# Kernel optimization log

Hardware: AMD Instinct MI355X
Metric: run time of the kernel (lower is better)

The kernel has to match this reference:

```python
import jax, jax.numpy as jnp
import numpy as np

B, CIN, COUT, HID, H, W, K, PAD = 16, 64, 64, 32, 32, 32, 5, 2


def self_attention(x, Wq, Wk, Wv):
    # x: [B,C,H,W]; Wq,Wk: [HID,C]; Wv: [C,C]  (1x1 convs as channel matmuls)
    b, c, h, w = x.shape
    n = h * w
    xf = x.reshape(b, c, n)                      # [B,C,N]
    q = jnp.einsum('dc,bcn->bdn', Wq, xf)        # [B,HID,N]
    k = jnp.einsum('dc,bcn->bdn', Wk, xf)        # [B,HID,N]
    v = jnp.einsum('ec,bcn->ben', Wv, xf)        # [B,C,N]
    scores = jnp.einsum('bdn,bdm->bnm', q, k)    # [B,N,N]
    attn = jax.nn.softmax(scores, axis=-1)
    out = jnp.einsum('bcm,bnm->bcn', v, attn)    # aggregate values
    out = out.reshape(b, c, h, w)
    return x + out, attn                          # residual


def conv_lstm_cell(x, h, c, W_lstm, b_lstm):
    combined = jnp.concatenate([x, h], axis=1)   # [B,CIN+COUT,H,W]
    gates = jax.lax.conv_general_dilated(
        combined, W_lstm, window_strides=(1, 1),
        padding=[(PAD, PAD), (PAD, PAD)],
        dimension_numbers=('NCHW', 'OIHW', 'NCHW'))
    gates = gates + b_lstm[None, :, None, None]
    i, f, o, g = jnp.split(gates, 4, axis=1)
    i, f, o = jax.nn.sigmoid(i), jax.nn.sigmoid(f), jax.nn.sigmoid(o)
    g = jnp.tanh(g)
    c_new = f * c + i * g
    h_new = o * jnp.tanh(c_new)
    return h_new, c_new


def setup_inputs() -> dict:
    key = jax.random.key(0)
    ks = jax.random.split(key, 12)
    s = 0.05
    return {
        'x': jax.random.normal(ks[0], (B, CIN, H, W), jnp.float32),
        'h': jax.random.normal(ks[1], (B, COUT, H, W), jnp.float32),
        'c': jax.random.normal(ks[2], (B, COUT, H, W), jnp.float32),
        'Wq_x': jax.random.normal(ks[3], (HID, CIN), jnp.float32) * s,
        'Wk_x': jax.random.normal(ks[4], (HID, CIN), jnp.float32) * s,
        'Wv_x': jax.random.normal(ks[5], (CIN, CIN), jnp.float32) * s,
        'Wq_h': jax.random.normal(ks[6], (HID, COUT), jnp.float32) * s,
        'Wk_h': jax.random.normal(ks[7], (HID, COUT), jnp.float32) * s,
        'Wv_h': jax.random.normal(ks[8], (COUT, COUT), jnp.float32) * s,
        'W_lstm': jax.random.normal(ks[9], (4 * COUT, CIN + COUT, K, K), jnp.float32) * s,
        'b_lstm': jnp.zeros((4 * COUT,), jnp.float32),
    }


def reference(x, h, c, Wq_x, Wk_x, Wv_x, Wq_h, Wk_h, Wv_h, W_lstm, b_lstm):
    X, _ = self_attention(x, Wq_x, Wk_x, Wv_x)
    new_h, new_c = conv_lstm_cell(X, h, c, W_lstm, b_lstm)
    new_h, atten = self_attention(new_h, Wq_h, Wk_h, Wv_h)
    new_h = new_h + new_h  # faithful to `new_h += new_h`
    return new_h, new_c, atten
```

## Files before the change

### kernel.cpp

```cpp
#include <hip/hip_runtime.h>
#include <hip/hip_bf16.h>
#include <cstddef>
#include <cstdint>

#define NTOK 1024
#define NB   16
#define NC   64
#define NHID 32

#define PAD_BSTRIDE 165888
#define PAD_KSTRIDE 82944
#define PAD_BYTES   5308416

typedef __attribute__((ext_vector_type(8))) short short8;
typedef __attribute__((ext_vector_type(4))) float f32x4;

__device__ __forceinline__ ushort f2b(float f) {
  uint32_t u = __builtin_bit_cast(uint32_t, f);
  return (ushort)((u + 0x7FFFu + ((u >> 16) & 1u)) >> 16);
}
__device__ __forceinline__ float b2f(ushort u) {
  return __builtin_bit_cast(float, (uint32_t)u << 16);
}

__global__ __launch_bounds__(256) void tpose_bf16_kernel(
    const float* __restrict__ src, ushort* __restrict__ dst, int padded) {
  __shared__ float tile[64][65];
  int t = threadIdx.x;
  int n0 = blockIdx.x * 64, b = blockIdx.y;
  const float* s = src + (size_t)b * NC * NTOK;
#pragma unroll
  for (int r = 0; r < 4; ++r) {
    int c = r * 16 + (t >> 4);
    int nl = (t & 15) * 4;
    float4 v = *(const float4*)(s + (size_t)c * NTOK + n0 + nl);
    tile[c][nl] = v.x; tile[c][nl + 1] = v.y; tile[c][nl + 2] = v.z; tile[c][nl + 3] = v.w;
  }
  __syncthreads();
  int tok = t >> 2, c0 = (t & 3) * 16;
  __attribute__((aligned(16))) ushort tmp[16];
#pragma unroll
  for (int i = 0; i < 16; ++i) tmp[i] = f2b(tile[c0 + i][tok]);
  int gtok = n0 + tok;
  ushort* d;
  if (padded)
    d = dst + (size_t)b * PAD_BSTRIDE + ((gtok >> 5) + 2) * 2304 + ((gtok & 31) + 2) * 64 + c0;
  else
    d = dst + ((size_t)b * NTOK + gtok) * NC + c0;
  *(uint4*)(d)     = *(const uint4*)(tmp);
  *(uint4*)(d + 8) = *(const uint4*)(tmp + 8);
}

__global__ __launch_bounds__(256) void wqkv_pre_kernel(
    const float* __restrict__ Wq, const float* __restrict__ Wk,
    const float* __restrict__ Wv, ushort* __restrict__ wqb,
    ushort* __restrict__ wkb, ushort* __restrict__ wvb) {
  int i = blockIdx.x * 256 + threadIdx.x;
  if (i < 2048) { wqb[i] = f2b(Wq[i]); wkb[i] = f2b(Wk[i]); }
  wvb[i] = f2b(Wv[i]);
}

__global__ __launch_bounds__(256) void qkvproj_kernel(
    const ushort* __restrict__ xT, const ushort* __restrict__ wqb,
    const ushort* __restrict__ wkb, const ushort* __restrict__ wvb,
    ushort* __restrict__ qT, ushort* __restrict__ kT, ushort* __restrict__ vb) {
  __shared__ ushort sq[64][32], sk[64][32];
  int t = threadIdx.x, wave = t >> 6, lane = t & 63;
  int lo = lane & 15, lg = lane >> 4;
  int n0 = blockIdx.x * 64, b = blockIdx.y;
  int nw = n0 + wave * 16;
  const ushort* xrow = xT + ((size_t)b * NTOK + nw + lo) * NC + 8 * lg;
  short8 a0 = *(const short8*)(xrow);
  short8 a1 = *(const short8*)(xrow + 32);
  f32x4 aq[2], ak[2];
#pragma unroll
  for (int dg = 0; dg < 2; ++dg) {
    const ushort* wq = wqb + (size_t)(dg * 16 + lo) * NC + 8 * lg;
    const ushort* wk = wkb + (size_t)(dg * 16 + lo) * NC + 8 * lg;
    f32x4 z = {0.f, 0.f, 0.f, 0.f};
    aq[dg] = __builtin_amdgcn_mfma_f32_16x16x32_bf16(a0, *(const short8*)(wq), z, 0, 0, 0);
    aq[dg] = __builtin_amdgcn_mfma_f32_16x16x32_bf16(a1, *(const short8*)(wq + 32), aq[dg], 0, 0, 0);
    ak[dg] = __builtin_amdgcn_mfma_f32_16x16x32_bf16(a0, *(const short8*)(wk), z, 0, 0, 0);
    ak[dg] = __builtin_amdgcn_mfma_f32_16x16x32_bf16(a1, *(const short8*)(wk + 32), ak[dg], 0, 0, 0);
  }
  f32x4 av[4];
#pragma unroll
  for (int g = 0; g < 4; ++g) {
    const ushort* wv = wvb + (size_t)(g * 16 + lo) * NC + 8 * lg;
    f32x4 z = {0.f, 0.f, 0.f, 0.f};
    av[g] = __builtin_amdgcn_mfma_f32_16x16x32_bf16(*(const short8*)(wv), a0, z, 0, 0, 0);
    av[g] = __builtin_amdgcn_mfma_f32_16x16x32_bf16(*(const short8*)(wv + 32), a1, av[g], 0, 0, 0);
  }
#pragma unroll
  for (int dg = 0; dg < 2; ++dg)
#pragma unroll
    for (int r = 0; r < 4; ++r) {
      sq[wave * 16 + 4 * lg + r][dg * 16 + lo] = f2b(aq[dg][r]);
      sk[wave * 16 + 4 * lg + r][dg * 16 + lo] = f2b(ak[dg][r]);
    }
  ushort* vbase = vb + (size_t)b * NC * NTOK + nw + lo;
#pragma unroll
  for (int g = 0; g < 4; ++g)
#pragma unroll
    for (int r = 0; r < 4; ++r)
      vbase[(size_t)(g * 16 + lg * 4 + r) * NTOK] = f2b(av[g][r]);
  __syncthreads();
  int tok = t >> 2, d0 = (t & 3) * 8;
  size_t base = ((size_t)b * NTOK + n0 + tok) * NHID + d0;
  *(short8*)(qT + base) = *(const short8*)(&sq[tok][d0]);
  *(short8*)(kT + base) = *(const short8*)(&sk[tok][d0]);
}

#define SP 1048
template <bool ATTN2>
__global__ __launch_bounds__(256) void attn_fused_kernel(
    const ushort* __restrict__ qT, const ushort* __restrict__ kT,
    const ushort* __restrict__ vb, const float* __restrict__ resid,
    float* __restrict__ attnf, float* __restrict__ outf,
    ushort* __restrict__ outb_pad, float scale) {
  __shared__ ushort s_lds[16 * SP];
  __shared__ float wmax[4][16], wsum[4][16];
  int t = threadIdx.x, wave = t >> 6, lane = t & 63;
  int lo = lane & 15, lg = lane >> 4;
  int n0 = blockIdx.x * 16, b = blockIdx.y;
  int m0 = wave * 256;
  short8 a = *(const short8*)(qT + ((size_t)b * NTOK + n0 + lo) * NHID + 8 * lg);
  f32x4 acc[16];
#pragma unroll
  for (int j = 0; j < 16; ++j) {
    short8 bf = *(const short8*)(kT + ((size_t)b * NTOK + m0 + j * 16 + lo) * NHID + 8 * lg);
    f32x4 z = {0.f, 0.f, 0.f, 0.f};
    acc[j] = __builtin_amdgcn_mfma_f32_16x16x32_bf16(a, bf, z, 0, 0, 0);
  }
  float pm[4];
#pragma unroll
  for (int r = 0; r < 4; ++r) {
    float m = acc[0][r];
#pragma unroll
    for (int j = 1; j < 16; ++j) m = fmaxf(m, acc[j][r]);
#pragma unroll
    for (int off = 1; off < 16; off <<= 1) m = fmaxf(m, __shfl_xor(m, off, 64));
    pm[r] = m;
  }
  if (lo == 0)
#pragma unroll
    for (int r = 0; r < 4; ++r) wmax[wave][4 * lg + r] = pm[r];
  __syncthreads();
  float mr[4];
#pragma unroll
  for (int r = 0; r < 4; ++r)
    mr[r] = fmaxf(fmaxf(wmax[0][4 * lg + r], wmax[1][4 * lg + r]),
                  fmaxf(wmax[2][4 * lg + r], wmax[3][4 * lg + r]));
  float ps[4] = {0.f, 0.f, 0.f, 0.f};
#pragma unroll
  for (int j = 0; j < 16; ++j)
#pragma unroll
    for (int r = 0; r < 4; ++r) {
      float e = __expf(acc[j][r] - mr[r]);
      acc[j][r] = e;
      ps[r] += e;
    }
#pragma unroll
  for (int r = 0; r < 4; ++r)
#pragma unroll
    for (int off = 1; off < 16; off <<= 1) ps[r] += __shfl_xor(ps[r], off, 64);
  if (lo == 0)
#pragma unroll
    for (int r = 0; r < 4; ++r) wsum[wave][4 * lg + r] = ps[r];
  __syncthreads();
  float inv[4];
#pragma unroll
  for (int r = 0; r < 4; ++r)
    inv[r] = 1.f / (wsum[0][4 * lg + r] + wsum[1][4 * lg + r] +
                    wsum[2][4 * lg + r] + wsum[3][4 * lg + r]);
#pragma unroll
  for (int j = 0; j < 16; ++j)
#pragma unroll
    for (int r = 0; r < 4; ++r)
      s_lds[(4 * lg + r) * SP + m0 + j * 16 + lo] = f2b(acc[j][r] * inv[r]);
  __syncthreads();
  if constexpr (ATTN2) {
    int ml = lane * 4;
    float* abase = attnf + ((size_t)b * NTOK + n0) * NTOK + m0;
#pragma unroll
    for (int n = 0; n < 16; ++n) {
      ushort4 sv = *(const ushort4*)(s_lds + n * SP + m0 + ml);
      float4 o;
      o.x = b2f(sv.x); o.y = b2f(sv.y); o.z = b2f(sv.z); o.w = b2f(sv.w);
      *(float4*)(abase + (size_t)n * NTOK + ml) = o;
    }
  }
  int cb = wave * 16;
  const ushort* vbb = vb + ((size_t)b * NC + cb + lo) * NTOK;
  f32x4 acc2 = {0.f, 0.f, 0.f, 0.f}, acc3 = {0.f, 0.f, 0.f, 0.f};
  for (int ms = 0; ms < NTOK; ms += 64) {
    short8 af0 = *(const short8*)(s_lds + lo * SP + ms + 8 * lg);
    short8 bf0 = *(const short8*)(vbb + ms + 8 * lg);
    short8 af1 = *(const short8*)(s_lds + lo * SP + ms + 32 + 8 * lg);
    short8 bf1 = *(const short8*)(vbb + ms + 32 + 8 * lg);
    acc2 = __builtin_amdgcn_mfma_f32_16x16x32_bf16(af0, bf0, acc2, 0, 0, 0);
    acc3 = __builtin_amdgcn_mfma_f32_16x16x32_bf16(af1, bf1, acc3, 0, 0, 0);
  }
#pragma unroll
  for (int r = 0; r < 4; ++r) acc2[r] += acc3[r];
  int c = cb + lo;
  float4 rv = *(const float4*)(resid + ((size_t)b * NC + c) * NTOK + n0 + 4 * lg);
  float rvv[4] = {rv.x, rv.y, rv.z, rv.w};
  if constexpr (ATTN2) {
    float4 o;
    o.x = scale * (rvv[0] + acc2[0]); o.y = scale * (rvv[1] + acc2[1]);
    o.z = scale * (rvv[2] + acc2[2]); o.w = scale * (rvv[3] + acc2[3]);
    *(float4*)(outf + ((size_t)b * NC + c) * NTOK + n0 + 4 * lg) = o;
  } else {
#pragma unroll
    for (int r = 0; r < 4; ++r) {
      int tok = n0 + 4 * lg + r;
      float val = scale * (rvv[r] + acc2[r]);
      outb_pad[(size_t)b * PAD_BSTRIDE + ((tok >> 5) + 2) * 2304 +
               ((tok & 31) + 2) * 64 + c] = f2b(val);
    }
  }
}

__global__ __launch_bounds__(256) void wpre_kernel(
    const float* __restrict__ W, ushort* __restrict__ Wb) {
  int idx = blockIdx.x * 256 + threadIdx.x;
  int oc = idx >> 7, ic = idx & 127;
  const float* src = W + (size_t)idx * 25;
#pragma unroll
  for (int kk = 0; kk < 25; ++kk)
    Wb[((size_t)oc * 25 + kk) * 128 + ic] = f2b(src[kk]);
}

#define AP 76
#define BP 76
__global__ __launch_bounds__(512, 1) void conv_mfma_kernel(
    const ushort* __restrict__ pad,
    const ushort* __restrict__ Wb,
    float* __restrict__ gates0, float* __restrict__ gates1) {
  __shared__ ushort ldsA[2][256 * AP];
  __shared__ ushort ldsB[288 * BP];
  int t = threadIdx.x;
  int lane = t & 63, lo = lane & 15, lg = lane >> 4;
  int wid = t >> 6, oc_g = wid & 3, px_g = wid >> 2;
  int rp = blockIdx.x, kh = blockIdx.y, b = blockIdx.z;
  const ushort* padKH = pad + (size_t)b * PAD_BSTRIDE + (size_t)kh * PAD_KSTRIDE
                        + (size_t)(rp * 4) * 2304;

  for (int i = t; i < 2304; i += 512) {
    int pxw = i >> 3, ch8 = (i & 7) * 8;
    uint4 v = *(const uint4*)(padKH + (size_t)pxw * 64 + ch8);
    *(uint4*)(ldsB + pxw * BP + ch8) = v;
  }

  const ushort *wsrc0, *wsrc1, *wsrc2, *wsrc3;
  int adst0, adst1, adst2, adst3;
  {
    int i0 = t, i1 = 512 + t, i2 = 1024 + t, i3 = 1536 + t;
    wsrc0 = Wb + (size_t)(i0 >> 3) * 3200 + kh * 64 + (i0 & 7) * 8;
    wsrc1 = Wb + (size_t)(i1 >> 3) * 3200 + kh * 64 + (i1 & 7) * 8;
    wsrc2 = Wb + (size_t)(i2 >> 3) * 3200 + kh * 64 + (i2 & 7) * 8;
    wsrc3 = Wb + (size_t)(i3 >> 3) * 3200 + kh * 64 + (i3 & 7) * 8;
    adst0 = (i0 >> 3) * AP + (i0 & 7) * 8;
    adst1 = (i1 >> 3) * AP + (i1 & 7) * 8;
    adst2 = (i2 >> 3) * AP + (i2 & 7) * 8;
    adst3 = (i3 >> 3) * AP + (i3 & 7) * 8;
  }
  uint4 w0 = *(const uint4*)(wsrc0);
  uint4 w1 = *(const uint4*)(wsrc1);
  uint4 w2 = *(const uint4*)(wsrc2);
  uint4 w3 = *(const uint4*)(wsrc3);

  f32x4 acc[4][4];
#pragma unroll
  for (int i = 0; i < 4; ++i)
#pragma unroll
    for (int j = 0; j < 4; ++j) acc[i][j] = {0.f, 0.f, 0.f, 0.f};

  __syncthreads();
  *(uint4*)(&ldsA[0][adst0]) = w0;
  *(uint4*)(&ldsA[0][adst1]) = w1;
  *(uint4*)(&ldsA[0][adst2]) = w2;
  *(uint4*)(&ldsA[0][adst3]) = w3;
  w0 = *(const uint4*)(wsrc0 + 128);
  w1 = *(const uint4*)(wsrc1 + 128);
  w2 = *(const uint4*)(wsrc2 + 128);
  w3 = *(const uint4*)(wsrc3 + 128);
  __syncthreads();

  for (int kk = 0; kk < 25; ++kk) {
    int cur = kk & 1;
    if (kk < 24) {
      int nxt = cur ^ 1;
      *(uint4*)(&ldsA[nxt][adst0]) = w0;
      *(uint4*)(&ldsA[nxt][adst1]) = w1;
      *(uint4*)(&ldsA[nxt][adst2]) = w2;
      *(uint4*)(&ldsA[nxt][adst3]) = w3;
      int kkn = (kk < 23) ? kk + 2 : 24;
      w0 = *(const uint4*)(wsrc0 + kkn * 128);
      w1 = *(const uint4*)(wsrc1 + kkn * 128);
      w2 = *(const uint4*)(wsrc2 + kkn * 128);
      w3 = *(const uint4*)(wsrc3 + kkn * 128);
    }
    int ky = kk / 5, kx = kk - 5 * ky;
    int tapoff = (ky * 36 + kx) * BP;
#pragma unroll
    for (int icc = 0; icc < 2; ++icc) {
      short8 af[4], bf[4];
#pragma unroll
      for (int i = 0; i < 4; ++i)
        af[i] = *(const short8*)(&ldsA[cur][(oc_g * 64 + i * 16 + lo) * AP + icc * 32 + 8 * lg]);
#pragma unroll
      for (int j = 0; j < 4; ++j) {
        int pxw = (px_g * 2 + (j >> 1)) * 36 + (j & 1) * 16 + lo;
        bf[j] = *(const short8*)(ldsB + tapoff + pxw * BP + icc * 32 + 8 * lg);
      }
#pragma unroll
      for (int i = 0; i < 4; ++i)
#pragma unroll
        for (int j = 0; j < 4; ++j)
          acc[i][j] = __builtin_amdgcn_mfma_f32_16x16x32_bf16(af[i], bf[j], acc[i][j], 0, 0, 0);
    }
    __syncthreads();
  }

  float* gp = kh ? gates1 : gates0;
#pragma unroll
  for (int i = 0; i < 4; ++i)
#pragma unroll
    for (int j = 0; j < 4; ++j)
#pragma unroll
      for (int r = 0; r < 4; ++r) {
        int oc = oc_g * 64 + i * 16 + lg * 4 + r;
        int p  = rp * 128 + px_g * 64 + j * 16 + lo;
        gp[(size_t)(b * 256 + oc) * NTOK + p] = acc[i][j][r];
      }
}

__global__ __launch_bounds__(256) void lstm_kernel(
    const float* __restrict__ g0, const float* __restrict__ g1,
    const float* __restrict__ bias, const float* __restrict__ c_in,
    float* __restrict__ c_out, float* __restrict__ h_out) {
  size_t idx = (size_t)blockIdx.x * 256 + threadIdx.x;
  size_t b = idx >> 16;
  size_t r = idx & 65535;
  int ocr = (int)(r >> 10);
  size_t gbo = b * (size_t)(256 * NTOK);
  float iv = g0[gbo + r]          + g1[gbo + r]          + bias[ocr];
  float fv = g0[gbo + 65536 + r]  + g1[gbo + 65536 + r]  + bias[64 + ocr];
  float ov = g0[gbo + 131072 + r] + g1[gbo + 131072 + r] + bias[128 + ocr];
  float gv = g0[gbo + 196608 + r] + g1[gbo + 196608 + r] + bias[192 + ocr];
  iv = 1.f / (1.f + expf(-iv));
  fv = 1.f / (1.f + expf(-fv));
  ov = 1.f / (1.f + expf(-ov));
  gv = tanhf(gv);
  float cn = fv * c_in[idx] + iv * gv;
  c_out[idx] = cn;
  h_out[idx] = ov * tanhf(cn);
}

extern "C" void kernel_launch(void* const* d_in, const int* in_sizes, int n_in,
                              void* d_out, int out_size, void* d_ws, size_t ws_size,
                              hipStream_t stream) {
  const float* x      = (const float*)d_in[0];
  const float* h      = (const float*)d_in[1];
  const float* c      = (const float*)d_in[2];
  const float* Wq_x   = (const float*)d_in[3];
  const float* Wk_x   = (const float*)d_in[4];
  const float* Wv_x   = (const float*)d_in[5];
  const float* Wq_h   = (const float*)d_in[6];
  const float* Wk_h   = (const float*)d_in[7];
  const float* Wv_h   = (const float*)d_in[8];
  const float* W_lstm = (const float*)d_in[9];
  const float* b_lstm = (const float*)d_in[10];

  float* out   = (float*)d_out;
  float* new_h = out;
  float* new_c = out + 1048576;
  float* atten = out + 2097152;

  ushort* wsu = (ushort*)d_ws;
  ushort* qT  = wsu;
  ushort* kT  = wsu + 524288;
  ushort* vb  = wsu + 1048576;
  ushort* xT  = wsu + 2097152;
  ushort* wqb = wsu + 3145728;
  ushort* wkb = wsu + 3147776;
  ushort* wvb = wsu + 3149824;

  float*  gates0 = atten;
  float*  gates1 = atten + 4194304;
  ushort* Wb     = (ushort*)(atten + 8388608);
  ushort* pad    = (ushort*)(atten + 9437184);
  float*  h_mid  = new_h;

  dim3 blk(256);
  hipMemsetAsync(pad, 0, PAD_BYTES, stream);
  tpose_bf16_kernel<<<dim3(16, NB), blk, 0, stream>>>(x, xT, 0);
  wqkv_pre_kernel<<<16, blk, 0, stream>>>(Wq_x, Wk_x, Wv_x, wqb, wkb, wvb);
  qkvproj_kernel<<<dim3(16, NB), blk, 0, stream>>>(xT, wqb, wkb, wvb, qT, kT, vb);
  attn_fused_kernel<false><<<dim3(64, NB), blk, 0, stream>>>(
      qT, kT, vb, x, nullptr, nullptr, pad , 1.0f);
  wpre_kernel<<<128, blk, 0, stream>>>(W_lstm, Wb);
  tpose_bf16_kernel<<<dim3(16, NB), blk, 0, stream>>>(h, pad + PAD_KSTRIDE, 1);
  conv_mfma_kernel<<<dim3(8, 2, NB), 512, 0, stream>>>(pad, Wb, gates0, gates1);
  lstm_kernel<<<4096, blk, 0, stream>>>(gates0, gates1, b_lstm, c, new_c, h_mid);
  tpose_bf16_kernel<<<dim3(16, NB), blk, 0, stream>>>(h_mid, xT, 0);
  wqkv_pre_kernel<<<16, blk, 0, stream>>>(Wq_h, Wk_h, Wv_h, wqb, wkb, wvb);
  qkvproj_kernel<<<dim3(16, NB), blk, 0, stream>>>(xT, wqb, wkb, wvb, qT, kT, vb);
  attn_fused_kernel<true><<<dim3(64, NB), blk, 0, stream>>>(
      qT, kT, vb, h_mid, atten, new_h, nullptr, 2.0f);
}
```

Measured before the change: 131.5 us.

## Fuse LSTM gating into conv kernel and fold transpose/weight cast into QKV projection

The conv kernel now covers both input halves (x-attention and h) in one 50-step K loop over a two-row pixel tile, and applies bias, sigmoid/tanh and the cell update in its epilogue. This removes the two gate buffers and the separate LSTM kernel. The QKV projection kernel now transposes and casts its fp32 input and weights itself, which removes the transpose and weight-precast launches. The trade-off is a larger LDS footprint for the B tile, and the conv grid changes from 8x2 to 16 tiles per batch with half the pixel work per block. The fast exp-based activations may differ slightly in precision.

```diff
diff --git a/kernel.cpp b/kernel.cpp
--- a/kernel.cpp
+++ b/kernel.cpp
@@ -22,9 +22,23 @@
 __device__ __forceinline__ float b2f(ushort u) {
   return __builtin_bit_cast(float, (uint32_t)u << 16);
 }
-
-__global__ __launch_bounds__(256) void tpose_bf16_kernel(
-    const float* __restrict__ src, ushort* __restrict__ dst, int padded) {
+__device__ __forceinline__ short8 ldw8(const float* __restrict__ p) {
+  float4 f0 = *(const float4*)p, f1 = *(const float4*)(p + 4);
+  short8 r;
+  r[0] = (short)f2b(f0.x); r[1] = (short)f2b(f0.y);
+  r[2] = (short)f2b(f0.z); r[3] = (short)f2b(f0.w);
+  r[4] = (short)f2b(f1.x); r[5] = (short)f2b(f1.y);
+  r[6] = (short)f2b(f1.z); r[7] = (short)f2b(f1.w);
+  return r;
+}
+__device__ __forceinline__ float sigm(float x) { return 1.f / (1.f + __expf(-x)); }
+__device__ __forceinline__ float tanh_fast(float x) {
+  float e = __expf(2.f * x);
+  return 1.f - 2.f / (e + 1.f);
+}
+
+__global__ __launch_bounds__(256) void tpose_pad_kernel(
+    const float* __restrict__ src, ushort* __restrict__ dst) {
   __shared__ float tile[64][65];
   int t = threadIdx.x;
   int n0 = blockIdx.x * 64, b = blockIdx.y;
@@ -42,54 +56,64 @@
 #pragma unroll
   for (int i = 0; i < 16; ++i) tmp[i] = f2b(tile[c0 + i][tok]);
   int gtok = n0 + tok;
-  ushort* d;
-  if (padded)
-    d = dst + (size_t)b * PAD_BSTRIDE + ((gtok >> 5) + 2) * 2304 + ((gtok & 31) + 2) * 64 + c0;
-  else
-    d = dst + ((size_t)b * NTOK + gtok) * NC + c0;
+  ushort* d = dst + (size_t)b * PAD_BSTRIDE +
+              ((gtok >> 5) + 2) * 2304 + ((gtok & 31) + 2) * 64 + c0;
   *(uint4*)(d)     = *(const uint4*)(tmp);
   *(uint4*)(d + 8) = *(const uint4*)(tmp + 8);
 }
 
-__global__ __launch_bounds__(256) void wqkv_pre_kernel(
-    const float* __restrict__ Wq, const float* __restrict__ Wk,
-    const float* __restrict__ Wv, ushort* __restrict__ wqb,
-    ushort* __restrict__ wkb, ushort* __restrict__ wvb) {
-  int i = blockIdx.x * 256 + threadIdx.x;
-  if (i < 2048) { wqb[i] = f2b(Wq[i]); wkb[i] = f2b(Wk[i]); }
-  wvb[i] = f2b(Wv[i]);
-}
-
 __global__ __launch_bounds__(256) void qkvproj_kernel(
-    const ushort* __restrict__ xT, const ushort* __restrict__ wqb,
-    const ushort* __restrict__ wkb, const ushort* __restrict__ wvb,
+    const float* __restrict__ x, const float* __restrict__ Wq,
+    const float* __restrict__ Wk, const float* __restrict__ Wv,
     ushort* __restrict__ qT, ushort* __restrict__ kT, ushort* __restrict__ vb) {
+  __shared__ float tile[64][65];
+  __shared__ ushort xb[64][72];
   __shared__ ushort sq[64][32], sk[64][32];
   int t = threadIdx.x, wave = t >> 6, lane = t & 63;
   int lo = lane & 15, lg = lane >> 4;
   int n0 = blockIdx.x * 64, b = blockIdx.y;
-  int nw = n0 + wave * 16;
-  const ushort* xrow = xT + ((size_t)b * NTOK + nw + lo) * NC + 8 * lg;
+  const float* s = x + (size_t)b * NC * NTOK;
+#pragma unroll
+  for (int r = 0; r < 4; ++r) {
+    int c = r * 16 + (t >> 4);
+    int nl = (t & 15) * 4;
+    float4 v = *(const float4*)(s + (size_t)c * NTOK + n0 + nl);
+    tile[c][nl] = v.x; tile[c][nl + 1] = v.y; tile[c][nl + 2] = v.z; tile[c][nl + 3] = v.w;
+  }
+  __syncthreads();
+  {
+    int tok = t >> 2, c0 = (t & 3) * 16;
+    __attribute__((aligned(16))) ushort tmp[16];
+#pragma unroll
+    for (int i = 0; i < 16; ++i) tmp[i] = f2b(tile[c0 + i][tok]);
+    *(uint4*)(&xb[tok][c0])     = *(const uint4*)(tmp);
+    *(uint4*)(&xb[tok][c0 + 8]) = *(const uint4*)(tmp + 8);
+  }
+  __syncthreads();
+  const ushort* xrow = &xb[wave * 16 + lo][8 * lg];
   short8 a0 = *(const short8*)(xrow);
   short8 a1 = *(const short8*)(xrow + 32);
   f32x4 aq[2], ak[2];
 #pragma unroll
   for (int dg = 0; dg < 2; ++dg) {
-    const ushort* wq = wqb + (size_t)(dg * 16 + lo) * NC + 8 * lg;
-    const ushort* wk = wkb + (size_t)(dg * 16 + lo) * NC + 8 * lg;
+    short8 wq0 = ldw8(Wq + (size_t)(dg * 16 + lo) * NC + 8 * lg);
+    short8 wq1 = ldw8(Wq + (size_t)(dg * 16 + lo) * NC + 32 + 8 * lg);
+    short8 wk0 = ldw8(Wk + (size_t)(dg * 16 + lo) * NC + 8 * lg);
+    short8 wk1 = ldw8(Wk + (size_t)(dg * 16 + lo) * NC + 32 + 8 * lg);
     f32x4 z = {0.f, 0.f, 0.f, 0.f};
-    aq[dg] = __builtin_amdgcn_mfma_f32_16x16x32_bf16(a0, *(const short8*)(wq), z, 0, 0, 0);
-    aq[dg] = __builtin_amdgcn_mfma_f32_16x16x32_bf16(a1, *(const short8*)(wq + 32), aq[dg], 0, 0, 0);
-    ak[dg] = __builtin_amdgcn_mfma_f32_16x16x32_bf16(a0, *(const short8*)(wk), z, 0, 0, 0);
-    ak[dg] = __builtin_amdgcn_mfma_f32_16x16x32_bf16(a1, *(const short8*)(wk + 32), ak[dg], 0, 0, 0);
+    aq[dg] = __builtin_amdgcn_mfma_f32_16x16x32_bf16(a0, wq0, z, 0, 0, 0);
+    aq[dg] = __builtin_amdgcn_mfma_f32_16x16x32_bf16(a1, wq1, aq[dg], 0, 0, 0);
+    ak[dg] = __builtin_amdgcn_mfma_f32_16x16x32_bf16(a0, wk0, z, 0, 0, 0);
+    ak[dg] = __builtin_amdgcn_mfma_f32_16x16x32_bf16(a1, wk1, ak[dg], 0, 0, 0);
   }
   f32x4 av[4];
 #pragma unroll
   for (int g = 0; g < 4; ++g) {
-    const ushort* wv = wvb + (size_t)(g * 16 + lo) * NC + 8 * lg;
+    short8 wv0 = ldw8(Wv + (size_t)(g * 16 + lo) * NC + 8 * lg);
+    short8 wv1 = ldw8(Wv + (size_t)(g * 16 + lo) * NC + 32 + 8 * lg);
     f32x4 z = {0.f, 0.f, 0.f, 0.f};
-    av[g] = __builtin_amdgcn_mfma_f32_16x16x32_bf16(*(const short8*)(wv), a0, z, 0, 0, 0);
-    av[g] = __builtin_amdgcn_mfma_f32_16x16x32_bf16(*(const short8*)(wv + 32), a1, av[g], 0, 0, 0);
+    av[g] = __builtin_amdgcn_mfma_f32_16x16x32_bf16(wv0, a0, z, 0, 0, 0);
+    av[g] = __builtin_amdgcn_mfma_f32_16x16x32_bf16(wv1, a1, av[g], 0, 0, 0);
   }
 #pragma unroll
   for (int dg = 0; dg < 2; ++dg)
@@ -98,7 +122,7 @@
       sq[wave * 16 + 4 * lg + r][dg * 16 + lo] = f2b(aq[dg][r]);
       sk[wave * 16 + 4 * lg + r][dg * 16 + lo] = f2b(ak[dg][r]);
     }
-  ushort* vbase = vb + (size_t)b * NC * NTOK + nw + lo;
+  ushort* vbase = vb + (size_t)b * NC * NTOK + n0 + wave * 16 + lo;
 #pragma unroll
   for (int g = 0; g < 4; ++g)
 #pragma unroll
@@ -225,42 +249,42 @@
 __global__ __launch_bounds__(256) void wpre_kernel(
     const float* __restrict__ W, ushort* __restrict__ Wb) {
   int idx = blockIdx.x * 256 + threadIdx.x;
-  int oc = idx >> 7, ic = idx & 127;
   const float* src = W + (size_t)idx * 25;
 #pragma unroll
   for (int kk = 0; kk < 25; ++kk)
-    Wb[((size_t)oc * 25 + kk) * 128 + ic] = f2b(src[kk]);
+    Wb[((size_t)(idx >> 7) * 25 + kk) * 128 + (idx & 127)] = f2b(src[kk]);
 }
 
 #define AP 76
 #define BP 76
-__global__ __launch_bounds__(512, 1) void conv_mfma_kernel(
+__global__ __launch_bounds__(512, 1) void conv_lstm_kernel(
     const ushort* __restrict__ pad,
     const ushort* __restrict__ Wb,
-    float* __restrict__ gates0, float* __restrict__ gates1) {
+    const float* __restrict__ bias, const float* __restrict__ c_in,
+    float* __restrict__ c_out, float* __restrict__ h_out) {
   __shared__ ushort ldsA[2][256 * AP];
-  __shared__ ushort ldsB[288 * BP];
+  __shared__ ushort ldsB[432 * BP];
   int t = threadIdx.x;
   int lane = t & 63, lo = lane & 15, lg = lane >> 4;
-  int wid = t >> 6, oc_g = wid & 3, px_g = wid >> 2;
-  int rp = blockIdx.x, kh = blockIdx.y, b = blockIdx.z;
-  const ushort* padKH = pad + (size_t)b * PAD_BSTRIDE + (size_t)kh * PAD_KSTRIDE
-                        + (size_t)(rp * 4) * 2304;
-
-  for (int i = t; i < 2304; i += 512) {
-    int pxw = i >> 3, ch8 = (i & 7) * 8;
-    uint4 v = *(const uint4*)(padKH + (size_t)pxw * 64 + ch8);
-    *(uint4*)(ldsB + pxw * BP + ch8) = v;
-  }
-
+  int wid = t >> 6, ocr_base = (wid & 3) * 16, ph = wid >> 2;
+  int pt = blockIdx.x, b = blockIdx.y;
+  {
+    const ushort* pb = pad + (size_t)b * PAD_BSTRIDE + (size_t)(pt * 2) * 2304;
+    for (int i = t; i < 432 * 8; i += 512) {
+      int pxw = i >> 3, ch8 = (i & 7) * 8;
+      int kh = pxw >= 216, w = pxw - kh * 216;
+      uint4 v = *(const uint4*)(pb + (size_t)kh * PAD_KSTRIDE + w * 64 + ch8);
+      *(uint4*)(ldsB + pxw * BP + ch8) = v;
+    }
+  }
   const ushort *wsrc0, *wsrc1, *wsrc2, *wsrc3;
   int adst0, adst1, adst2, adst3;
   {
     int i0 = t, i1 = 512 + t, i2 = 1024 + t, i3 = 1536 + t;
-    wsrc0 = Wb + (size_t)(i0 >> 3) * 3200 + kh * 64 + (i0 & 7) * 8;
-    wsrc1 = Wb + (size_t)(i1 >> 3) * 3200 + kh * 64 + (i1 & 7) * 8;
-    wsrc2 = Wb + (size_t)(i2 >> 3) * 3200 + kh * 64 + (i2 & 7) * 8;
-    wsrc3 = Wb + (size_t)(i3 >> 3) * 3200 + kh * 64 + (i3 & 7) * 8;
+    wsrc0 = Wb + (size_t)(i0 >> 3) * 3200 + (i0 & 7) * 8;
+    wsrc1 = Wb + (size_t)(i1 >> 3) * 3200 + (i1 & 7) * 8;
+    wsrc2 = Wb + (size_t)(i2 >> 3) * 3200 + (i2 & 7) * 8;
+    wsrc3 = Wb + (size_t)(i3 >> 3) * 3200 + (i3 & 7) * 8;
     adst0 = (i0 >> 3) * AP + (i0 & 7) * 8;
     adst1 = (i1 >> 3) * AP + (i1 & 7) * 8;
     adst2 = (i2 >> 3) * AP + (i2 & 7) * 8;
@@ -271,11 +295,11 @@
   uint4 w2 = *(const uint4*)(wsrc2);
   uint4 w3 = *(const uint4*)(wsrc3);
 
-  f32x4 acc[4][4];
+  f32x4 acc[4][2];
 #pragma unroll
   for (int i = 0; i < 4; ++i)
 #pragma unroll
-    for (int j = 0; j < 4; ++j) acc[i][j] = {0.f, 0.f, 0.f, 0.f};
+    for (int j = 0; j < 2; ++j) acc[i][j] = {0.f, 0.f, 0.f, 0.f};
 
   __syncthreads();
   *(uint4*)(&ldsA[0][adst0]) = w0;
@@ -288,75 +312,58 @@
   w3 = *(const uint4*)(wsrc3 + 128);
   __syncthreads();
 
-  for (int kk = 0; kk < 25; ++kk) {
-    int cur = kk & 1;
-    if (kk < 24) {
+  for (int s = 0; s < 50; ++s) {
+    int cur = s & 1;
+    if (s < 49) {
       int nxt = cur ^ 1;
       *(uint4*)(&ldsA[nxt][adst0]) = w0;
       *(uint4*)(&ldsA[nxt][adst1]) = w1;
       *(uint4*)(&ldsA[nxt][adst2]) = w2;
       *(uint4*)(&ldsA[nxt][adst3]) = w3;
-      int kkn = (kk < 23) ? kk + 2 : 24;
-      w0 = *(const uint4*)(wsrc0 + kkn * 128);
-      w1 = *(const uint4*)(wsrc1 + kkn * 128);
-      w2 = *(const uint4*)(wsrc2 + kkn * 128);
-      w3 = *(const uint4*)(wsrc3 + kkn * 128);
-    }
-    int ky = kk / 5, kx = kk - 5 * ky;
-    int tapoff = (ky * 36 + kx) * BP;
+      int s2 = (s < 48) ? s + 2 : 49;
+      int koff = (s2 < 25) ? s2 * 128 : (s2 - 25) * 128 + 64;
+      w0 = *(const uint4*)(wsrc0 + koff);
+      w1 = *(const uint4*)(wsrc1 + koff);
+      w2 = *(const uint4*)(wsrc2 + koff);
+      w3 = *(const uint4*)(wsrc3 + koff);
+    }
+    int kh = (s >= 25);
+    int tap = s - kh * 25;
+    int ky = tap / 5, kx = tap - 5 * ky;
+    int bbase = (kh * 216 + ky * 36 + kx) * BP;
 #pragma unroll
     for (int icc = 0; icc < 2; ++icc) {
-      short8 af[4], bf[4];
+      short8 af[4], bf[2];
 #pragma unroll
       for (int i = 0; i < 4; ++i)
-        af[i] = *(const short8*)(&ldsA[cur][(oc_g * 64 + i * 16 + lo) * AP + icc * 32 + 8 * lg]);
-#pragma unroll
-      for (int j = 0; j < 4; ++j) {
-        int pxw = (px_g * 2 + (j >> 1)) * 36 + (j & 1) * 16 + lo;
-        bf[j] = *(const short8*)(ldsB + tapoff + pxw * BP + icc * 32 + 8 * lg);
-      }
+        af[i] = *(const short8*)(&ldsA[cur][(i * 64 + ocr_base + lo) * AP + icc * 32 + 8 * lg]);
+#pragma unroll
+      for (int j = 0; j < 2; ++j)
+        bf[j] = *(const short8*)(ldsB + bbase + (ph * 36 + j * 16 + lo) * BP + icc * 32 + 8 * lg);
 #pragma unroll
       for (int i = 0; i < 4; ++i)
 #pragma unroll
-        for (int j = 0; j < 4; ++j)
+        for (int j = 0; j < 2; ++j)
           acc[i][j] = __builtin_amdgcn_mfma_f32_16x16x32_bf16(af[i], bf[j], acc[i][j], 0, 0, 0);
     }
     __syncthreads();
   }
 
-  float* gp = kh ? gates1 : gates0;
-#pragma unroll
-  for (int i = 0; i < 4; ++i)
-#pragma unroll
-    for (int j = 0; j < 4; ++j)
-#pragma unroll
-      for (int r = 0; r < 4; ++r) {
-        int oc = oc_g * 64 + i * 16 + lg * 4 + r;
-        int p  = rp * 128 + px_g * 64 + j * 16 + lo;
-        gp[(size_t)(b * 256 + oc) * NTOK + p] = acc[i][j][r];
-      }
-}
-
-__global__ __launch_bounds__(256) void lstm_kernel(
-    const float* __restrict__ g0, const float* __restrict__ g1,
-    const float* __restrict__ bias, const float* __restrict__ c_in,
-    float* __restrict__ c_out, float* __restrict__ h_out) {
-  size_t idx = (size_t)blockIdx.x * 256 + threadIdx.x;
-  size_t b = idx >> 16;
-  size_t r = idx & 65535;
-  int ocr = (int)(r >> 10);
-  size_t gbo = b * (size_t)(256 * NTOK);
-  float iv = g0[gbo + r]          + g1[gbo + r]          + bias[ocr];
-  float fv = g0[gbo + 65536 + r]  + g1[gbo + 65536 + r]  + bias[64 + ocr];
-  float ov = g0[gbo + 131072 + r] + g1[gbo + 131072 + r] + bias[128 + ocr];
-  float gv = g0[gbo + 196608 + r] + g1[gbo + 196608 + r] + bias[192 + ocr];
-  iv = 1.f / (1.f + expf(-iv));
-  fv = 1.f / (1.f + expf(-fv));
-  ov = 1.f / (1.f + expf(-ov));
-  gv = tanhf(gv);
-  float cn = fv * c_in[idx] + iv * gv;
-  c_out[idx] = cn;
-  h_out[idx] = ov * tanhf(cn);
+#pragma unroll
+  for (int j = 0; j < 2; ++j)
+#pragma unroll
+    for (int r = 0; r < 4; ++r) {
+      int ocr = ocr_base + lg * 4 + r;
+      int p = pt * 64 + ph * 32 + j * 16 + lo;
+      size_t ci = ((size_t)b * NC + ocr) * NTOK + p;
+      float iv = sigm(acc[0][j][r] + bias[ocr]);
+      float fv = sigm(acc[1][j][r] + bias[64 + ocr]);
+      float ov = sigm(acc[2][j][r] + bias[128 + ocr]);
+      float gv = tanh_fast(acc[3][j][r] + bias[192 + ocr]);
+      float cn = fv * c_in[ci] + iv * gv;
+      c_out[ci] = cn;
+      h_out[ci] = ov * tanh_fast(cn);
+    }
 }
 
 extern "C" void kernel_launch(void* const* d_in, const int* in_sizes, int n_in,
@@ -383,31 +390,20 @@
   ushort* qT  = wsu;
   ushort* kT  = wsu + 524288;
   ushort* vb  = wsu + 1048576;
-  ushort* xT  = wsu + 2097152;
-  ushort* wqb = wsu + 3145728;
-  ushort* wkb = wsu + 3147776;
-  ushort* wvb = wsu + 3149824;
-
-  float*  gates0 = atten;
-  float*  gates1 = atten + 4194304;
-  ushort* Wb     = (ushort*)(atten + 8388608);
-  ushort* pad    = (ushort*)(atten + 9437184);
-  float*  h_mid  = new_h;
+
+  ushort* Wb    = (ushort*)(atten + 8388608);
+  ushort* pad   = (ushort*)(atten + 9437184);
+  float*  h_mid = new_h;
 
   dim3 blk(256);
   hipMemsetAsync(pad, 0, PAD_BYTES, stream);
-  tpose_bf16_kernel<<<dim3(16, NB), blk, 0, stream>>>(x, xT, 0);
-  wqkv_pre_kernel<<<16, blk, 0, stream>>>(Wq_x, Wk_x, Wv_x, wqb, wkb, wvb);
-  qkvproj_kernel<<<dim3(16, NB), blk, 0, stream>>>(xT, wqb, wkb, wvb, qT, kT, vb);
+  qkvproj_kernel<<<dim3(16, NB), blk, 0, stream>>>(x, Wq_x, Wk_x, Wv_x, qT, kT, vb);
   attn_fused_kernel<false><<<dim3(64, NB), blk, 0, stream>>>(
       qT, kT, vb, x, nullptr, nullptr, pad , 1.0f);
   wpre_kernel<<<128, blk, 0, stream>>>(W_lstm, Wb);
-  tpose_bf16_kernel<<<dim3(16, NB), blk, 0, stream>>>(h, pad + PAD_KSTRIDE, 1);
-  conv_mfma_kernel<<<dim3(8, 2, NB), 512, 0, stream>>>(pad, Wb, gates0, gates1);
-  lstm_kernel<<<4096, blk, 0, stream>>>(gates0, gates1, b_lstm, c, new_c, h_mid);
-  tpose_bf16_kernel<<<dim3(16, NB), blk, 0, stream>>>(h_mid, xT, 0);
-  wqkv_pre_kernel<<<16, blk, 0, stream>>>(Wq_h, Wk_h, Wv_h, wqb, wkb, wvb);
-  qkvproj_kernel<<<dim3(16, NB), blk, 0, stream>>>(xT, wqb, wkb, wvb, qT, kT, vb);
+  tpose_pad_kernel<<<dim3(16, NB), blk, 0, stream>>>(h, pad + PAD_KSTRIDE);
+  conv_lstm_kernel<<<dim3(16, NB), 512, 0, stream>>>(pad, Wb, b_lstm, c, new_c, h_mid);
+  qkvproj_kernel<<<dim3(16, NB), blk, 0, stream>>>(h_mid, Wq_h, Wk_h, Wv_h, qT, kT, vb);
   attn_fused_kernel<true><<<dim3(64, NB), blk, 0, stream>>>(
       qT, kT, vb, h_mid, atten, new_h, nullptr, 2.0f);
 }
```

Result: no change. 129.5 us (-1.5%).
